# Performance work log

Measured on AMD Instinct MI355X. Metric: run time of the kernel, lower is better.

Reference implementation:

```python
import jax, jax.numpy as jnp
import numpy as np

INPUT_H = 512
INPUT_W = 512
POOL = 5
BN_EPS = 1e-5


def setup_inputs() -> dict:
    key = jax.random.key(0)
    ks = jax.random.split(key, 8)
    B = 16
    c3 = jax.random.normal(ks[0], (B, 512, 64, 64), jnp.float32)
    c4 = jax.random.normal(ks[1], (B, 1024, 32, 32), jnp.float32)
    xy = jax.random.uniform(ks[2], (B, 10, 4), jnp.float32) * 512.0
    # ensure x1<=x2, y1<=y2 like real detector boxes
    boxes = jnp.concatenate([jnp.minimum(xy[..., :2], xy[..., 2:]),
                             jnp.maximum(xy[..., :2], xy[..., 2:])], axis=-1)
    w_conv = jax.random.normal(ks[3], (512, 1536), jnp.float32) * 0.02  # 1x1 conv kernel
    b_conv = jnp.zeros((512,), jnp.float32)
    bn_gamma = jnp.ones((512,), jnp.float32)
    bn_beta = jnp.zeros((512,), jnp.float32)
    bn_mean = jax.random.normal(ks[4], (512,), jnp.float32) * 0.1
    bn_var = jax.random.uniform(ks[5], (512,), jnp.float32) * 0.5 + 0.5
    return {"c3": c3, "c4": c4, "boxes": boxes, "w_conv": w_conv, "b_conv": b_conv,
            "bn_gamma": bn_gamma, "bn_beta": bn_beta, "bn_mean": bn_mean, "bn_var": bn_var}


def _bin_weights(lo, hi, size, nout):
    """Adaptive-avg-pool bin weights over axis of length `size` for crop [lo,hi).
    Returns [nout, size] row-stochastic matrix (same math as AdaptiveAvgPool1d bins)."""
    length = hi - lo
    k = jnp.arange(nout)
    starts = lo + (k * length) // nout                      # floor(k*L/n)
    ends = lo + ((k + 1) * length + nout - 1) // nout        # ceil((k+1)*L/n)
    idx = jnp.arange(size)
    mask = (idx[None, :] >= starts[:, None]) & (idx[None, :] < ends[:, None])
    return mask.astype(jnp.float32) / (ends - starts)[:, None].astype(jnp.float32)


def reference(c3, c4, boxes, w_conv, b_conv, bn_gamma, bn_beta, bn_mean, bn_var):
    B = c3.shape[0]
    c4u = jax.image.resize(c4, (B, c4.shape[1], c4.shape[2] * 2, c4.shape[3] * 2),
                           method='bilinear')
    fused = jnp.concatenate([c3, c4u], axis=1)               # [B,1536,H,W]
    y = jnp.einsum('bchw,oc->bohw', fused, w_conv) + b_conv[None, :, None, None]
    inv = bn_gamma / jnp.sqrt(bn_var + BN_EPS)               # eval-mode BN
    y = y * inv[None, :, None, None] + (bn_beta - bn_mean * inv)[None, :, None, None]
    attr_blob = jax.nn.relu(y)                               # [B,512,H,W]
    H, W = attr_blob.shape[-2:]
    sx = W / INPUT_W
    sy = H / INPUT_H

    def pool_one(feat, box):  # feat [C,H,W], box [4] -> [C,5,5]
        x1 = jnp.clip(jnp.floor(box[0] * sx), 0, W - 1).astype(jnp.int32)
        y1 = jnp.clip(jnp.floor(box[1] * sy), 0, H - 1).astype(jnp.int32)
        x2 = jnp.clip(jnp.ceil(box[2] * sx), 0, W - 1).astype(jnp.int32)
        y2 = jnp.clip(jnp.ceil(box[3] * sy), 0, H - 1).astype(jnp.int32)
        x2 = jnp.where(x2 <= x1, jnp.minimum(x1 + 1, W), x2)
        y2 = jnp.where(y2 <= y1, jnp.minimum(y1 + 1, H), y2)
        wy = _bin_weights(y1, y2, H, POOL)                   # [5,H]
        wx = _bin_weights(x1, x2, W, POOL)                   # [5,W]
        return jnp.einsum('ph,chw,qw->cpq', wy, feat, wx)

    obj_blob = jax.vmap(lambda f, bx: jax.vmap(lambda b: pool_one(f, b))(bx))(attr_blob, boxes)
    return boxes, obj_blob  # ([B,10,4], [B,10,512,5,5])
```

## Files before the change

kernel.cpp:

```cpp
#include <hip/hip_runtime.h>
#include <stdint.h>

#define FH 64
#define FW 64
#define CIN 1536
#define C3C 512
#define C4C 1024
#define COUT 512
#define BATCH 16
#define NPIX 4096
#define NBOX 10
#define MPAD 256

typedef float v4f __attribute__((ext_vector_type(4)));

#define GLOAD_LDS16(g, l) __builtin_amdgcn_global_load_lds( \
    (const __attribute__((address_space(1))) void*)(g),     \
    (__attribute__((address_space(3))) void*)(l), 16, 0, 0)

__device__ __forceinline__ uint32_t pack4_fp8(float a, float b, float c, float d) {
    int lo = __builtin_amdgcn_cvt_pk_fp8_f32(a, b, 0, false);
    int v  = __builtin_amdgcn_cvt_pk_fp8_f32(c, d, lo, true);
    return (uint32_t)v;
}
__device__ __forceinline__ unsigned char f32_to_fp8(float a) {
    return (unsigned char)(__builtin_amdgcn_cvt_pk_fp8_f32(a, a, 0, false) & 0xff);
}

__global__ void prep_bn(const float* __restrict__ bng, const float* __restrict__ bnb,
                        const float* __restrict__ bnm, const float* __restrict__ bnv,
                        const float* __restrict__ bconv,
                        float* __restrict__ scale, float* __restrict__ shift) {
    int o = threadIdx.x;
    if (o < COUT) {
        float inv = bng[o] / sqrtf(bnv[o] + 1e-5f);
        scale[o] = inv * 0.0625f;
        shift[o] = bnb[o] + inv * (bconv[o] - bnm[o]);
    }
}

__global__ void conv_w(const float* __restrict__ w, uint32_t* __restrict__ w8, int n4) {
    int i = blockIdx.x * 256 + threadIdx.x;
    if (i < n4) {
        float4 f = *(const float4*)(w + i * 4);
        w8[i] = pack4_fp8(f.x * 16.0f, f.y * 16.0f, f.z * 16.0f, f.w * 16.0f);
    }
}

__global__ __launch_bounds__(256) void build_fusedT(const float* __restrict__ c3,
                                                    const float* __restrict__ c4,
                                                    unsigned char* __restrict__ fusedT) {
    __shared__ uint32_t lds[64 * 36];
    int ct = blockIdx.x;
    int y  = blockIdx.y;
    int b  = blockIdx.z;
    int t  = threadIdx.x;
    int pg = t & 15;
    int cq = t >> 4;

    #pragma unroll
    for (int r = 0; r < 2; ++r) {
        int cquad = cq + 16 * r;
        float vv[4][4];
        if (ct < 4) {
            int ch = ct * 128 + 4 * cquad;
            const float* src = c3 + (((size_t)(b * C3C + ch) * FH + y) * FW) + 4 * pg;
            #pragma unroll
            for (int k = 0; k < 4; ++k) {
                float4 f = *(const float4*)(src + (size_t)k * (FH * FW));
                vv[k][0] = f.x; vv[k][1] = f.y; vv[k][2] = f.z; vv[k][3] = f.w;
            }
        } else {
            int ch = ct * 128 - 512 + 4 * cquad;
            int jy = y >> 1;
            int jyB = min(max(jy + ((y & 1) ? 1 : -1), 0), 31);
            int k0 = 2 * pg;
            int km = max(k0 - 1, 0), kp = min(k0 + 2, 31);
            const float* base = c4 + (size_t)(b * C4C + ch) * 1024;
            #pragma unroll
            for (int k = 0; k < 4; ++k) {
                const float* pc = base + (size_t)k * 1024;
                const float* r0 = pc + jy * 32;
                const float* r1 = pc + jyB * 32;
                float rbm = 0.75f * r0[km]     + 0.25f * r1[km];
                float rb0 = 0.75f * r0[k0]     + 0.25f * r1[k0];
                float rb1 = 0.75f * r0[k0 + 1] + 0.25f * r1[k0 + 1];
                float rbp = 0.75f * r0[kp]     + 0.25f * r1[kp];
                vv[k][0] = 0.75f * rb0 + 0.25f * rbm;
                vv[k][1] = 0.75f * rb0 + 0.25f * rb1;
                vv[k][2] = 0.75f * rb1 + 0.25f * rb0;
                vv[k][3] = 0.75f * rb1 + 0.25f * rbp;
            }
        }
        #pragma unroll
        for (int i = 0; i < 4; ++i)
            lds[(4 * pg + i) * 36 + cquad] = pack4_fp8(vv[0][i], vv[1][i], vv[2][i], vv[3][i]);
    }
    __syncthreads();
    int g = t & 7;
    #pragma unroll
    for (int rr = 0; rr < 2; ++rr) {
        int px = (t >> 3) + 32 * rr;
        uint4 w = *(const uint4*)(&lds[px * 36 + 4 * g]);
        *(uint4*)(fusedT + ((size_t)b * NPIX + y * FW + px) * CIN + ct * 128 + g * 16) = w;
    }
}

__global__ __launch_bounds__(256) void gemm_bn_relu(
        const unsigned char* __restrict__ w8,
        const unsigned char* __restrict__ fusedT,
        const float* __restrict__ scale, const float* __restrict__ shift,
        unsigned char* __restrict__ attr) {
    __shared__ __align__(16) unsigned char lds_a[128 * 64];
    __shared__ __align__(16) unsigned char lds_b[128 * 64];
    int t  = threadIdx.x;
    int n0 = blockIdx.x * 128;
    int o0 = blockIdx.y * 128;
    int b  = blockIdx.z;
    int wave = t >> 6, lane = t & 63;
    int wm = wave & 1, wn = wave >> 1;
    int quad = lane >> 4, l16 = lane & 15;
    const unsigned char* fb = fusedT + (size_t)b * NPIX * CIN;

    v4f acc[4][4];
    #pragma unroll
    for (int i = 0; i < 4; ++i)
        #pragma unroll
        for (int j = 0; j < 4; ++j) acc[i][j] = (v4f)0.0f;

    int row = t >> 2;
    int cg  = (t & 3) ^ ((row >> 1) & 3);
    const unsigned char* ga0 = w8 + (size_t)(o0 + row) * CIN + cg * 16;
    const unsigned char* ga1 = w8 + (size_t)(o0 + row + 64) * CIN + cg * 16;
    const unsigned char* gb0 = fb + (size_t)(n0 + row) * CIN + cg * 16;
    const unsigned char* gb1 = fb + (size_t)(n0 + row + 64) * CIN + cg * 16;
    unsigned char* la0 = lds_a + t * 16;
    unsigned char* la1 = lds_a + 4096 + t * 16;
    unsigned char* lb0 = lds_b + t * 16;
    unsigned char* lb1 = lds_b + 4096 + t * 16;

    int ra[4], rb[4];
    #pragma unroll
    for (int i = 0; i < 4; ++i) { ra[i] = wm * 64 + i * 16 + l16; rb[i] = wn * 64 + i * 16 + l16; }
    int q2 = quad >> 1, q1 = (quad & 1) * 8;

    for (int kt = 0; kt < CIN / 64; ++kt) {
        __syncthreads();
        GLOAD_LDS16(ga0, la0);
        GLOAD_LDS16(ga1, la1);
        GLOAD_LDS16(gb0, lb0);
        GLOAD_LDS16(gb1, lb1);
        ga0 += 64; ga1 += 64; gb0 += 64; gb1 += 64;
        __syncthreads();

        #pragma unroll
        for (int s = 0; s < 2; ++s) {
            long af[4], bf[4];
            #pragma unroll
            for (int i = 0; i < 4; ++i) {
                int pa = (2 * s + q2) ^ ((ra[i] >> 1) & 3);
                af[i] = *(const long*)(lds_a + ra[i] * 64 + pa * 16 + q1);
                int pb = (2 * s + q2) ^ ((rb[i] >> 1) & 3);
                bf[i] = *(const long*)(lds_b + rb[i] * 64 + pb * 16 + q1);
            }
            #pragma unroll
            for (int i = 0; i < 4; ++i)
                #pragma unroll
                for (int j = 0; j < 4; ++j)
                    acc[i][j] = __builtin_amdgcn_mfma_f32_16x16x32_fp8_fp8(af[i], bf[j], acc[i][j], 0, 0, 0);
        }
    }

    unsigned char* ab = attr + (size_t)b * COUT * NPIX;
    #pragma unroll
    for (int i = 0; i < 4; ++i) {
        int obase = o0 + wm * 64 + i * 16 + quad * 4;
        #pragma unroll
        for (int r = 0; r < 4; ++r) {
            int oo = obase + r;
            float sc = scale[oo], sh = shift[oo];
            #pragma unroll
            for (int j = 0; j < 4; ++j) {
                int n = n0 + wn * 64 + j * 16 + l16;
                float v = fmaxf(acc[i][j][r] * sc + sh, 0.0f);
                ab[(size_t)oo * NPIX + n] = f32_to_fp8(v);
            }
        }
    }
}

__global__ __launch_bounds__(256) void build_P(const float* __restrict__ boxes,
                                               unsigned char* __restrict__ P) {
    int br  = blockIdx.x;
    int m25 = blockIdx.y;
    int b   = br / NBOX;
    int m   = (br % NBOX) * 25 + m25;
    int p   = m25 / 5, q = m25 % 5;
    int t   = threadIdx.x;
    int y   = t >> 2;
    int x0  = (t & 3) * 16;
    const float* bx = boxes + (size_t)br * 4;
    int x1 = min(max((int)floorf(bx[0] * 0.125f), 0), 63);
    int y1 = min(max((int)floorf(bx[1] * 0.125f), 0), 63);
    int x2 = min(max((int)ceilf (bx[2] * 0.125f), 0), 63);
    int y2 = min(max((int)ceilf (bx[3] * 0.125f), 0), 63);
    if (x2 <= x1) x2 = min(x1 + 1, 64);
    if (y2 <= y1) y2 = min(y1 + 1, 64);
    int Lx = x2 - x1, Ly = y2 - y1;
    int sx = x1 + (q * Lx) / 5;
    int ex = x1 + ((q + 1) * Lx + 4) / 5;
    int sy = y1 + (p * Ly) / 5;
    int ey = y1 + ((p + 1) * Ly + 4) / 5;
    float wyv  = (y >= sy && y < ey) ? 1.0f / (float)(ey - sy) : 0.0f;
    float pval = 64.0f * wyv / (float)(ex - sx);
    float v[16];
    #pragma unroll
    for (int i = 0; i < 16; ++i) {
        int xi = x0 + i;
        v[i] = (xi >= sx && xi < ex) ? pval : 0.0f;
    }
    uint4 w;
    w.x = pack4_fp8(v[0],  v[1],  v[2],  v[3]);
    w.y = pack4_fp8(v[4],  v[5],  v[6],  v[7]);
    w.z = pack4_fp8(v[8],  v[9],  v[10], v[11]);
    w.w = pack4_fp8(v[12], v[13], v[14], v[15]);
    *(uint4*)(P + ((size_t)b * MPAD + m) * NPIX + y * FW + x0) = w;
}

__global__ __launch_bounds__(256) void pool_gemm(
        const unsigned char* __restrict__ P,
        const unsigned char* __restrict__ attr,
        float* __restrict__ part2) {
    __shared__ __align__(16) unsigned char lds_a[128 * 64];
    __shared__ __align__(16) unsigned char lds_b[128 * 64];
    int t  = threadIdx.x;
    int m0 = blockIdx.x * 128;
    int c0 = (blockIdx.y & 3) * 128;
    int seg = blockIdx.y >> 2;
    int b  = blockIdx.z;
    int wave = t >> 6, lane = t & 63;
    int wm = wave & 1, wn = wave >> 1;
    int quad = lane >> 4, l16 = lane & 15;
    const unsigned char* Pb = P + (size_t)b * MPAD * NPIX + seg * 1024;
    const unsigned char* ab = attr + (size_t)b * COUT * NPIX + seg * 1024;

    v4f acc[4][4];
    #pragma unroll
    for (int i = 0; i < 4; ++i)
        #pragma unroll
        for (int j = 0; j < 4; ++j) acc[i][j] = (v4f)0.0f;

    int row = t >> 2;
    int cg  = (t & 3) ^ ((row >> 1) & 3);
    const unsigned char* ga0 = Pb + (size_t)(m0 + row) * NPIX + cg * 16;
    const unsigned char* ga1 = Pb + (size_t)(m0 + row + 64) * NPIX + cg * 16;
    const unsigned char* gb0 = ab + (size_t)(c0 + row) * NPIX + cg * 16;
    const unsigned char* gb1 = ab + (size_t)(c0 + row + 64) * NPIX + cg * 16;
    unsigned char* la0 = lds_a + t * 16;
    unsigned char* la1 = lds_a + 4096 + t * 16;
    unsigned char* lb0 = lds_b + t * 16;
    unsigned char* lb1 = lds_b + 4096 + t * 16;

    int ra[4], rb[4];
    #pragma unroll
    for (int i = 0; i < 4; ++i) { ra[i] = wm * 64 + i * 16 + l16; rb[i] = wn * 64 + i * 16 + l16; }
    int q2 = quad >> 1, q1 = (quad & 1) * 8;

    for (int kt = 0; kt < 1024 / 64; ++kt) {
        __syncthreads();
        GLOAD_LDS16(ga0, la0);
        GLOAD_LDS16(ga1, la1);
        GLOAD_LDS16(gb0, lb0);
        GLOAD_LDS16(gb1, lb1);
        ga0 += 64; ga1 += 64; gb0 += 64; gb1 += 64;
        __syncthreads();

        #pragma unroll
        for (int s = 0; s < 2; ++s) {
            long af[4], bf[4];
            #pragma unroll
            for (int i = 0; i < 4; ++i) {
                int pa = (2 * s + q2) ^ ((ra[i] >> 1) & 3);
                af[i] = *(const long*)(lds_a + ra[i] * 64 + pa * 16 + q1);
                int pb = (2 * s + q2) ^ ((rb[i] >> 1) & 3);
                bf[i] = *(const long*)(lds_b + rb[i] * 64 + pb * 16 + q1);
            }
            #pragma unroll
            for (int i = 0; i < 4; ++i)
                #pragma unroll
                for (int j = 0; j < 4; ++j)
                    acc[i][j] = __builtin_amdgcn_mfma_f32_16x16x32_fp8_fp8(af[i], bf[j], acc[i][j], 0, 0, 0);
        }
    }

    float* pp = part2 + (((size_t)seg * BATCH + b) * MPAD) * COUT;
    #pragma unroll
    for (int i = 0; i < 4; ++i) {
        #pragma unroll
        for (int r = 0; r < 4; ++r) {
            int mrow = m0 + wm * 64 + i * 16 + quad * 4 + r;
            #pragma unroll
            for (int j = 0; j < 4; ++j) {
                int c = c0 + wn * 64 + j * 16 + l16;
                pp[(size_t)mrow * COUT + c] = acc[i][j][r];
            }
        }
    }
}

__global__ __launch_bounds__(256) void pool_reduce(const float* __restrict__ part2,
                                                   float* __restrict__ out) {
    const size_t SEG = (size_t)BATCH * MPAD * COUT;
    int i = blockIdx.x * 256 + threadIdx.x;
    int c = i & (COUT - 1);
    int m = (i >> 9) & (MPAD - 1);
    int b = i >> 17;
    if (m >= 250) return;
    float s = part2[i] + part2[i + SEG] + part2[i + 2 * SEG] + part2[i + 3 * SEG];
    int box = m / 25, bin = m - box * 25;
    out[640 + ((size_t)(b * NBOX + box) * COUT + c) * 25 + bin] = s * 0.015625f;
}

extern "C" void kernel_launch(void* const* d_in, const int* in_sizes, int n_in,
                              void* d_out, int out_size, void* d_ws, size_t ws_size,
                              hipStream_t stream) {
    const float* c3     = (const float*)d_in[0];
    const float* c4     = (const float*)d_in[1];
    const float* boxes  = (const float*)d_in[2];
    const float* w_conv = (const float*)d_in[3];
    const float* b_conv = (const float*)d_in[4];
    const float* bng    = (const float*)d_in[5];
    const float* bnb    = (const float*)d_in[6];
    const float* bnm    = (const float*)d_in[7];
    const float* bnv    = (const float*)d_in[8];
    float* out = (float*)d_out;

    char* ws = (char*)d_ws;
    unsigned char* fusedT = (unsigned char*)ws;
    unsigned char* P      = (unsigned char*)(ws + 100663296);
    float*         part2  = (float*)(ws + 117440512);
    unsigned char* w8     = (unsigned char*)(ws + 150994944);
    float*         scale  = (float*)(ws + 151781376);
    float*         shift  = (float*)(ws + 151783424);
    unsigned char* attr   = (unsigned char*)(ws + 151785472);

    hipMemcpyAsync(d_out, d_in[2], 640 * sizeof(float), hipMemcpyDeviceToDevice, stream);
    prep_bn<<<1, 512, 0, stream>>>(bng, bnb, bnm, bnv, b_conv, scale, shift);
    conv_w<<<(COUT * CIN / 4 + 255) / 256, 256, 0, stream>>>(w_conv, (uint32_t*)w8, COUT * CIN / 4);
    build_P<<<dim3(160, 25), 256, 0, stream>>>(boxes, P);
    build_fusedT<<<dim3(12, 64, 16), 256, 0, stream>>>(c3, c4, fusedT);
    gemm_bn_relu<<<dim3(32, 4, 16), 256, 0, stream>>>(w8, fusedT, scale, shift, attr);
    pool_gemm<<<dim3(2, 16, 16), 256, 0, stream>>>(P, attr, part2);
    pool_reduce<<<(BATCH * MPAD * COUT) / 256, 256, 0, stream>>>(part2, out);
    (void)in_sizes; (void)n_in; (void)out_size; (void)ws_size;
}
```

Measured before the change: 433.8 us.

## Rewrite FP8 GEMM as 256x256 tile with double-buffered LDS ping-pong pipeline

The 1x1 conv GEMM moves from a 128x128 tile with 256 threads and a single LDS buffer to a 256x256 tile with 512 threads (8 waves). It double-buffers LDS and interleaves async global-to-LDS loads of the next K-tile with four MFMA quadrants, raising wave priority around the MFMA bursts. The aim is to hide global load latency behind compute and raise arithmetic intensity per byte loaded. In exchange, the grid drops to 512 blocks, and the heavier register and LDS use (64 KB) may limit occupancy. The hand-written s_waitcnt and barrier choreography is also fragile.

```diff
diff --git a/kernel.cpp b/kernel.cpp
--- a/kernel.cpp
+++ b/kernel.cpp
@@ -11,12 +11,15 @@
 #define NPIX 4096
 #define NBOX 10
 #define MPAD 256
+#define NT 24
 
 typedef float v4f __attribute__((ext_vector_type(4)));
 
 #define GLOAD_LDS16(g, l) __builtin_amdgcn_global_load_lds( \
     (const __attribute__((address_space(1))) void*)(g),     \
     (__attribute__((address_space(3))) void*)(l), 16, 0, 0)
+
+#define BARRIER() asm volatile("s_barrier" ::: "memory")
 
 __device__ __forceinline__ uint32_t pack4_fp8(float a, float b, float c, float d) {
     int lo = __builtin_amdgcn_cvt_pk_fp8_f32(a, b, 0, false);
@@ -106,87 +109,140 @@
     }
 }
 
-__global__ __launch_bounds__(256) void gemm_bn_relu(
+__global__ __launch_bounds__(512, 2) void gemm_bn_relu(
         const unsigned char* __restrict__ w8,
         const unsigned char* __restrict__ fusedT,
         const float* __restrict__ scale, const float* __restrict__ shift,
         unsigned char* __restrict__ attr) {
-    __shared__ __align__(16) unsigned char lds_a[128 * 64];
-    __shared__ __align__(16) unsigned char lds_b[128 * 64];
-    int t  = threadIdx.x;
-    int n0 = blockIdx.x * 128;
-    int o0 = blockIdx.y * 128;
-    int b  = blockIdx.z;
-    int wave = t >> 6, lane = t & 63;
-    int wm = wave & 1, wn = wave >> 1;
-    int quad = lane >> 4, l16 = lane & 15;
+    __shared__ __align__(16) unsigned char lds_a[2][16384];
+    __shared__ __align__(16) unsigned char lds_b[2][16384];
+    const int t  = threadIdx.x;
+    const int n0 = blockIdx.x * 256;
+    const int o0 = blockIdx.y * 256;
+    const int b  = blockIdx.z;
+    const int wave = t >> 6, lane = t & 63;
+    const int wm = wave & 1, wn = wave >> 1;
+    const int quad = lane >> 4, l16 = lane & 15;
+    const int q2 = quad >> 1, q1 = (quad & 1) * 8;
+    const int keyq = (l16 >> 1) & 3;
+    const int cs0 = ((q2 ^ keyq) * 16) + q1;
+    const int cs1 = (((2 + q2) ^ keyq) * 16) + q1;
     const unsigned char* fb = fusedT + (size_t)b * NPIX * CIN;
 
-    v4f acc[4][4];
-    #pragma unroll
-    for (int i = 0; i < 4; ++i)
+    const int lrow = t >> 2;
+    const int cg   = (t & 3) ^ ((t >> 3) & 3);
+    const size_t gA0 = (size_t)(o0 + ((t >> 8) << 7) + (lrow & 63)) * CIN + cg * 16;
+    const size_t gB0 = (size_t)(n0 + (((t >> 7) & 3) << 6) + (lrow & 31)) * CIN + cg * 16;
+
+#define STAGE_A(tt, h, d) GLOAD_LDS16(w8 + gA0 + (size_t)(h) * (64 * CIN) + (size_t)(tt) * 64, \
+                                      &lds_a[d][(h) * 8192 + t * 16])
+#define STAGE_B(tt, h, d) GLOAD_LDS16(fb + gB0 + (size_t)(h) * (32 * CIN) + (size_t)(tt) * 64, \
+                                      &lds_b[d][(h) * 8192 + t * 16])
+#define RD_A(base, ih, i, csel) (*(const long*)((base) + (((ih) * 128 + wm * 64 + (i) * 16 + l16) << 6) + (csel)))
+#define RD_B(base, jh, j, csel) (*(const long*)((base) + (((jh) * 128 + wn * 32 + (j) * 16 + l16) << 6) + (csel)))
+
+    v4f acc[8][4];
+    #pragma unroll
+    for (int i = 0; i < 8; ++i)
         #pragma unroll
         for (int j = 0; j < 4; ++j) acc[i][j] = (v4f)0.0f;
 
-    int row = t >> 2;
-    int cg  = (t & 3) ^ ((row >> 1) & 3);
-    const unsigned char* ga0 = w8 + (size_t)(o0 + row) * CIN + cg * 16;
-    const unsigned char* ga1 = w8 + (size_t)(o0 + row + 64) * CIN + cg * 16;
-    const unsigned char* gb0 = fb + (size_t)(n0 + row) * CIN + cg * 16;
-    const unsigned char* gb1 = fb + (size_t)(n0 + row + 64) * CIN + cg * 16;
-    unsigned char* la0 = lds_a + t * 16;
-    unsigned char* la1 = lds_a + 4096 + t * 16;
-    unsigned char* lb0 = lds_b + t * 16;
-    unsigned char* lb1 = lds_b + 4096 + t * 16;
-
-    int ra[4], rb[4];
-    #pragma unroll
-    for (int i = 0; i < 4; ++i) { ra[i] = wm * 64 + i * 16 + l16; rb[i] = wn * 64 + i * 16 + l16; }
-    int q2 = quad >> 1, q1 = (quad & 1) * 8;
-
-    for (int kt = 0; kt < CIN / 64; ++kt) {
-        __syncthreads();
-        GLOAD_LDS16(ga0, la0);
-        GLOAD_LDS16(ga1, la1);
-        GLOAD_LDS16(gb0, lb0);
-        GLOAD_LDS16(gb1, lb1);
-        ga0 += 64; ga1 += 64; gb0 += 64; gb1 += 64;
-        __syncthreads();
-
-        #pragma unroll
-        for (int s = 0; s < 2; ++s) {
-            long af[4], bf[4];
-            #pragma unroll
-            for (int i = 0; i < 4; ++i) {
-                int pa = (2 * s + q2) ^ ((ra[i] >> 1) & 3);
-                af[i] = *(const long*)(lds_a + ra[i] * 64 + pa * 16 + q1);
-                int pb = (2 * s + q2) ^ ((rb[i] >> 1) & 3);
-                bf[i] = *(const long*)(lds_b + rb[i] * 64 + pb * 16 + q1);
-            }
+    STAGE_A(0, 0, 0); STAGE_B(0, 0, 0);
+    STAGE_A(0, 1, 0); STAGE_B(0, 1, 0);
+    STAGE_A(1, 0, 1); STAGE_B(1, 0, 1);
+    asm volatile("s_waitcnt vmcnt(2)" ::: "memory");
+    BARRIER();
+
+    long a0[4][2], a1[4][2], b0[2][2], b1[2][2];
+
+    for (int kt = 0; kt < NT; ++kt) {
+        const unsigned char* bA = lds_a[kt & 1];
+        const unsigned char* bB = lds_b[kt & 1];
+        const int cur = kt & 1, nxt = cur ^ 1;
+
+        #pragma unroll
+        for (int i = 0; i < 4; ++i) { a0[i][0] = RD_A(bA, 0, i, cs0); a0[i][1] = RD_A(bA, 0, i, cs1); }
+        #pragma unroll
+        for (int j = 0; j < 2; ++j) { b0[j][0] = RD_B(bB, 0, j, cs0); b0[j][1] = RD_B(bB, 0, j, cs1); }
+        if (kt + 1 < NT) STAGE_A(kt + 1, 1, nxt);
+        BARRIER();
+        __builtin_amdgcn_s_setprio(1);
+        #pragma unroll
+        for (int s = 0; s < 2; ++s)
             #pragma unroll
             for (int i = 0; i < 4; ++i)
                 #pragma unroll
-                for (int j = 0; j < 4; ++j)
-                    acc[i][j] = __builtin_amdgcn_mfma_f32_16x16x32_fp8_fp8(af[i], bf[j], acc[i][j], 0, 0, 0);
-        }
+                for (int j = 0; j < 2; ++j)
+                    acc[i][j] = __builtin_amdgcn_mfma_f32_16x16x32_fp8_fp8(a0[i][s], b0[j][s], acc[i][j], 0, 0, 0);
+        __builtin_amdgcn_s_setprio(0);
+        BARRIER();
+
+        #pragma unroll
+        for (int j = 0; j < 2; ++j) { b1[j][0] = RD_B(bB, 1, j, cs0); b1[j][1] = RD_B(bB, 1, j, cs1); }
+        if (kt + 1 < NT) STAGE_B(kt + 1, 1, nxt);
+        BARRIER();
+        __builtin_amdgcn_s_setprio(1);
+        #pragma unroll
+        for (int s = 0; s < 2; ++s)
+            #pragma unroll
+            for (int i = 0; i < 4; ++i)
+                #pragma unroll
+                for (int j = 0; j < 2; ++j)
+                    acc[i][2 + j] = __builtin_amdgcn_mfma_f32_16x16x32_fp8_fp8(a0[i][s], b1[j][s], acc[i][2 + j], 0, 0, 0);
+        __builtin_amdgcn_s_setprio(0);
+        BARRIER();
+
+        #pragma unroll
+        for (int i = 0; i < 4; ++i) { a1[i][0] = RD_A(bA, 1, i, cs0); a1[i][1] = RD_A(bA, 1, i, cs1); }
+        if (kt + 2 < NT) STAGE_A(kt + 2, 0, cur);
+        BARRIER();
+        __builtin_amdgcn_s_setprio(1);
+        #pragma unroll
+        for (int s = 0; s < 2; ++s)
+            #pragma unroll
+            for (int i = 0; i < 4; ++i)
+                #pragma unroll
+                for (int j = 0; j < 2; ++j)
+                    acc[4 + i][j] = __builtin_amdgcn_mfma_f32_16x16x32_fp8_fp8(a1[i][s], b0[j][s], acc[4 + i][j], 0, 0, 0);
+        __builtin_amdgcn_s_setprio(0);
+        BARRIER();
+
+        if (kt + 2 < NT) STAGE_B(kt + 2, 0, cur);
+        BARRIER();
+        __builtin_amdgcn_s_setprio(1);
+        #pragma unroll
+        for (int s = 0; s < 2; ++s)
+            #pragma unroll
+            for (int i = 0; i < 4; ++i)
+                #pragma unroll
+                for (int j = 0; j < 2; ++j)
+                    acc[4 + i][2 + j] = __builtin_amdgcn_mfma_f32_16x16x32_fp8_fp8(a1[i][s], b1[j][s], acc[4 + i][2 + j], 0, 0, 0);
+        __builtin_amdgcn_s_setprio(0);
+        if (kt < NT - 2) { asm volatile("s_waitcnt vmcnt(2)" ::: "memory"); }
+        else            { asm volatile("s_waitcnt vmcnt(0)" ::: "memory"); }
+        BARRIER();
     }
 
     unsigned char* ab = attr + (size_t)b * COUT * NPIX;
     #pragma unroll
-    for (int i = 0; i < 4; ++i) {
-        int obase = o0 + wm * 64 + i * 16 + quad * 4;
+    for (int a = 0; a < 8; ++a) {
+        int obase = o0 + wm * 128 + (a >> 2) * 64 + (a & 3) * 16 + quad * 4;
         #pragma unroll
         for (int r = 0; r < 4; ++r) {
             int oo = obase + r;
             float sc = scale[oo], sh = shift[oo];
             #pragma unroll
-            for (int j = 0; j < 4; ++j) {
-                int n = n0 + wn * 64 + j * 16 + l16;
-                float v = fmaxf(acc[i][j][r] * sc + sh, 0.0f);
+            for (int bb = 0; bb < 4; ++bb) {
+                int n = n0 + wn * 64 + (bb >> 1) * 32 + (bb & 1) * 16 + l16;
+                float v = fmaxf(acc[a][bb][r] * sc + sh, 0.0f);
                 ab[(size_t)oo * NPIX + n] = f32_to_fp8(v);
             }
         }
     }
+#undef STAGE_A
+#undef STAGE_B
+#undef RD_A
+#undef RD_B
 }
 
 __global__ __launch_bounds__(256) void build_P(const float* __restrict__ boxes,
@@ -349,7 +405,7 @@
     conv_w<<<(COUT * CIN / 4 + 255) / 256, 256, 0, stream>>>(w_conv, (uint32_t*)w8, COUT * CIN / 4);
     build_P<<<dim3(160, 25), 256, 0, stream>>>(boxes, P);
     build_fusedT<<<dim3(12, 64, 16), 256, 0, stream>>>(c3, c4, fusedT);
-    gemm_bn_relu<<<dim3(32, 4, 16), 256, 0, stream>>>(w8, fusedT, scale, shift, attr);
+    gemm_bn_relu<<<dim3(16, 2, 16), 512, 0, stream>>>(w8, fusedT, scale, shift, attr);
     pool_gemm<<<dim3(2, 16, 16), 256, 0, stream>>>(P, attr, part2);
     pool_reduce<<<(BATCH * MPAD * COUT) / 256, 256, 0, stream>>>(part2, out);
     (void)in_sizes; (void)n_in; (void)out_size; (void)ws_size;
```

Result: no change. 427.5 us (-1.4%).
